# Performance work log

Measured on AMD Instinct MI355X. Metric: run time of the kernel, lower is better.

## Reference

```python
import jax, jax.numpy as jnp
import numpy as np

HID, PROJ, ATTN = 512, 1024, 128
B, L = 4, 2048


def _apply_rope(x):
    # x: [B, L, 2, ATTN]; RoPE over sequence dim (axis=1)
    half = x.shape[-1] // 2
    inv_freq = jnp.power(10000.0, -jnp.arange(half, dtype=jnp.float32) / half)
    pos = jnp.arange(x.shape[1], dtype=x.dtype)
    sinusoid = pos[:, None] * inv_freq.astype(x.dtype)          # [L, half]
    sin = jnp.sin(sinusoid)[None, :, None, :]                   # [1, L, 1, half]
    cos = jnp.cos(sinusoid)[None, :, None, :]
    x1, x2 = jnp.split(x, 2, axis=-1)
    return jnp.concatenate([x1 * cos - x2 * sin, x2 * cos + x1 * sin], axis=-1)


def setup_inputs() -> dict:
    key = jax.random.key(0)
    ks = jax.random.split(key, 8)
    node = jax.random.normal(ks[0], (B, L, HID), dtype=jnp.float32)
    bias = jax.random.normal(ks[1], (B, L, L), dtype=jnp.float32)
    scaling = jnp.full((1,), ATTN ** -0.5, dtype=jnp.float32)
    w1 = jax.random.normal(ks[2], (HID, 2 * PROJ + ATTN), dtype=jnp.float32) * (HID ** -0.5)
    b1 = jnp.zeros((2 * PROJ + ATTN,), dtype=jnp.float32)
    ms_weight = jax.random.normal(ks[3], (2, ATTN), dtype=jnp.float32) * 0.02
    ms_bias = jnp.zeros((2, ATTN), dtype=jnp.float32)
    w2 = jax.random.normal(ks[4], (PROJ, HID), dtype=jnp.float32) * (PROJ ** -0.5)
    b2 = jnp.zeros((HID,), dtype=jnp.float32)
    return {"node": node, "bias": bias, "scaling": scaling, "w1": w1, "b1": b1,
            "ms_weight": ms_weight, "ms_bias": ms_bias, "w2": w2, "b2": b2}


def reference(node, bias, scaling, w1, b1, ms_weight, ms_bias, w2, b2):
    # gated projection + SiLU
    gva = jax.nn.silu(node @ w1 + b1)                           # [B, L, 2P+A]
    gates, values, base = jnp.split(gva, [PROJ, 2 * PROJ], axis=-1)
    # multi-headed scaling -> [B, L, 2, A], then RoPE, then split q/k
    qk = base[..., None, :] * ms_weight + ms_bias               # [B, L, 2, A]
    qk = _apply_rope(qk)
    q, k = qk[..., 0, :], qk[..., 1, :]                         # [B, L, A]
    logits = jnp.einsum('bid,bjd->bij', q * scaling, k) + bias  # [B, L, L]
    attn = jax.nn.softmax(logits, axis=-1)
    out = jnp.einsum('bij,bjd->bid', attn, values)              # [B, L, P]
    return (out * gates) @ w2 + b2                              # [B, L, HID]
```

## Files before the change

### kernel.cpp

```cpp
#include <hip/hip_runtime.h>
#include <math.h>

#define HIDN 512
#define PROJ 1024
#define ATTN 128
#define BATCH 4
#define SEQ 2048
#define N1 (2*PROJ+ATTN)
#define ROWS (BATCH*SEQ)
#define QR 16

typedef __attribute__((ext_vector_type(4))) float f32x4;
typedef __attribute__((ext_vector_type(8))) short bf16x8;

__device__ __forceinline__ short f2bf(float x){
    unsigned u = __builtin_bit_cast(unsigned, x);
    unsigned rounding = 0x7fffu + ((u >> 16) & 1u);
    u += rounding;
    return (short)(u >> 16);
}
__device__ __forceinline__ float bf2f(short s){
    unsigned u = ((unsigned)(unsigned short)s) << 16;
    return __builtin_bit_cast(float, u);
}

__device__ __forceinline__ void gload16(const void* g, void* l){
    __builtin_amdgcn_global_load_lds((const __attribute__((address_space(1))) void*)g,
                                     (__attribute__((address_space(3))) void*)l,
                                     16, 0, 0);
}

template<class Epi>
__device__ __forceinline__ void gemm_bt_tile(const short* __restrict__ A, int lda,
                                             const short* __restrict__ BT, int ldb,
                                             int m0, int n0, int K, Epi epi)
{
    __shared__ __align__(16) short lA[2][128*64];
    __shared__ __align__(16) short lB[2][128*64];
    const int t = threadIdx.x;
    const int lane = t & 63;
    const int w = t >> 6;
    const int wr = (w >> 1) * 64, wc = (w & 1) * 64;
    const int half = lane >> 4, l16 = lane & 15;

    f32x4 acc[4][4];
    #pragma unroll
    for (int i=0;i<4;i++)
        #pragma unroll
        for (int j=0;j<4;j++)
            acc[i][j] = (f32x4){0.f,0.f,0.f,0.f};

    auto stage = [&](int buf, int k0){
        #pragma unroll
        for (int i = 0; i < 4; i++) {
            int li = i*256 + t;
            int r = li >> 3, s = li & 7;
            int ss = s ^ (r & 7);
            gload16(A + (size_t)(m0+r)*lda + k0 + ss*8, lA[buf] + li*8);
        }
        #pragma unroll
        for (int i = 0; i < 4; i++) {
            int li = i*256 + t;
            int r = li >> 3, s = li & 7;
            int ss = s ^ (r & 7);
            gload16(BT + (size_t)(n0+r)*ldb + k0 + ss*8, lB[buf] + li*8);
        }
    };

    stage(0, 0);
    __syncthreads();
    int cur = 0;
    for (int k0 = 64; k0 <= K; k0 += 64) {
        if (k0 < K) stage(cur^1, k0);
        #pragma unroll
        for (int kk = 0; kk < 64; kk += 32) {
            bf16x8 af[4], bfr[4];
            const int cs = (kk >> 3) + half;
            #pragma unroll
            for (int i=0;i<4;i++){
                int row = wr + i*16 + l16;
                af[i] = *(const bf16x8*)(lA[cur] + row*64 + ((cs ^ (row & 7)) << 3));
            }
            #pragma unroll
            for (int j=0;j<4;j++){
                int row = wc + j*16 + l16;
                bfr[j] = *(const bf16x8*)(lB[cur] + row*64 + ((cs ^ (row & 7)) << 3));
            }
            #pragma unroll
            for (int i=0;i<4;i++)
                #pragma unroll
                for (int j=0;j<4;j++)
                    acc[i][j] = __builtin_amdgcn_mfma_f32_16x16x32_bf16(af[i], bfr[j], acc[i][j], 0, 0, 0);
        }
        __syncthreads();
        cur ^= 1;
    }
    #pragma unroll
    for (int i=0;i<4;i++)
        #pragma unroll
        for (int j=0;j<4;j++)
            #pragma unroll
            for (int q=0;q<4;q++)
                epi(m0 + wr + i*16 + half*4 + q, n0 + wc + j*16 + l16, acc[i][j][q]);
}

__global__ void k_cast_node(const float* __restrict__ in, short* __restrict__ out){
    int idx = blockIdx.x*256 + threadIdx.x;
    const float4 v = ((const float4*)in)[idx];
    short4 o; o.x = f2bf(v.x); o.y = f2bf(v.y); o.z = f2bf(v.z); o.w = f2bf(v.w);
    ((short4*)out)[idx] = o;
}

__global__ void k_transpose_cast(const float* __restrict__ in, short* __restrict__ out,
                                 int R, int C){
    __shared__ short tile[64][65];
    int r0 = blockIdx.y*64, c0 = blockIdx.x*64;
    int t = threadIdx.x;
    #pragma unroll
    for (int i=0;i<16;i++){
        int lin = i*256 + t; int r = lin>>6, c = lin&63;
        tile[r][c] = f2bf(in[(size_t)(r0+r)*C + c0+c]);
    }
    __syncthreads();
    #pragma unroll
    for (int i=0;i<16;i++){
        int lin = i*256 + t; int c = lin>>6, r = lin&63;
        out[(size_t)(c0+c)*R + r0+r] = tile[r][c];
    }
}

__global__ void k_transpose_v(const short* __restrict__ values, short* __restrict__ VT){
    __shared__ short tile[64][65];
    int z = blockIdx.z;
    int c0 = blockIdx.x*64, r0 = blockIdx.y*64;
    int t = threadIdx.x;
    #pragma unroll
    for (int i=0;i<16;i++){
        int lin = i*256 + t; int r = lin>>6, c = lin&63;
        tile[r][c] = values[(size_t)(z*SEQ + r0+r)*PROJ + c0+c];
    }
    __syncthreads();
    #pragma unroll
    for (int i=0;i<16;i++){
        int lin = i*256 + t; int c = lin>>6, r = lin&63;
        VT[((size_t)z*PROJ + c0+c)*SEQ + r0+r] = tile[r][c];
    }
}

__global__ __launch_bounds__(256) void k_mm1(const short* __restrict__ nodeb,
        const short* __restrict__ w1T, const float* __restrict__ b1,
        short* __restrict__ gates, short* __restrict__ values, short* __restrict__ baseb){
    int b = blockIdx.x;
    int wg = (b & 7) * (N1/128*64/8) + (b >> 3);
    int n0 = (wg % (N1/128))*128, m0 = (wg / (N1/128))*128;
    gemm_bt_tile(nodeb, HIDN, w1T, HIDN, m0, n0, HIDN,
        [=](int row, int col, float v){
            v += b1[col];
            v = v / (1.f + __expf(-v));
            short bv = f2bf(v);
            if (col < PROJ)        gates [(size_t)row*PROJ + col]        = bv;
            else if (col < 2*PROJ) values[(size_t)row*PROJ + col-PROJ]   = bv;
            else                   baseb [(size_t)row*ATTN + col-2*PROJ] = bv;
        });
}

__global__ void k_rope2(const short* __restrict__ baseb, const float* __restrict__ msw,
                        const float* __restrict__ msb, const float* __restrict__ scaling,
                        short* __restrict__ qb, short* __restrict__ kb){
    int idx = blockIdx.x*256 + threadIdx.x;
    int d = idx & 63;
    int row = idx >> 6;
    int l = row & (SEQ-1);
    float inv = exp2f(-(float)d * (13.287712379549449f/64.f));
    float ang = (float)l * inv;
    float s = sinf(ang), c = cosf(ang);
    const short* bp = baseb + (size_t)row*ATTN;
    float b_lo = bf2f(bp[d]), b_hi = bf2f(bp[d+64]);
    float x1q = b_lo*msw[d]        + msb[d];
    float x2q = b_hi*msw[d+64]     + msb[d+64];
    float x1k = b_lo*msw[128+d]    + msb[128+d];
    float x2k = b_hi*msw[128+d+64] + msb[128+d+64];
    float sc = scaling[0];
    qb[(size_t)row*ATTN + d]    = f2bf((x1q*c - x2q*s)*sc);
    qb[(size_t)row*ATTN + d+64] = f2bf((x2q*c + x1q*s)*sc);
    kb[(size_t)row*ATTN + d]    = f2bf(x1k*c - x2k*s);
    kb[(size_t)row*ATTN + d+64] = f2bf(x2k*c + x1k*s);
}

__global__ __launch_bounds__(512, 4) void k_qksm(
        const short* __restrict__ qg, const short* __restrict__ kg,
        const float* __restrict__ bias, short* __restrict__ P,
        float* __restrict__ linv)
{
    __shared__ float bt[2][16][260];
    __shared__ short pt[2][16][264];
    __shared__ float s_l[8][16];

    const int z = blockIdx.y;
    const int r0 = blockIdx.x * QR;
    const int t = threadIdx.x;
    const int w = t >> 6;
    const int lane = t & 63;
    const int l16 = lane & 15, half = lane >> 4;

    const short* Q  = qg + ((size_t)z*SEQ + r0)*ATTN;
    const short* K  = kg + (size_t)z*SEQ*ATTN;
    const float* Bb = bias + ((size_t)z*SEQ + r0)*SEQ;
    short* Pp = P + ((size_t)z*SEQ + r0)*SEQ;

    bf16x8 qf[4];
    #pragma unroll
    for (int kc=0;kc<4;kc++)
        qf[kc] = *(const bf16x8*)(Q + (size_t)l16*ATTN + kc*32 + half*8);

    const int brow = t >> 6, bcol = (t & 63)*4;
    f32x4 pra[2], prb[2];
    pra[0] = *(const f32x4*)(Bb + (size_t)brow*SEQ + bcol);
    prb[0] = *(const f32x4*)(Bb + (size_t)(8+brow)*SEQ + bcol);
    pra[1] = *(const f32x4*)(Bb + (size_t)brow*SEQ + 256 + bcol);
    prb[1] = *(const f32x4*)(Bb + (size_t)(8+brow)*SEQ + 256 + bcol);
    *(f32x4*)&bt[0][brow][bcol]   = pra[0];
    *(f32x4*)&bt[0][8+brow][bcol] = prb[0];
    __syncthreads();

    float ts = 0.f;
    #pragma unroll
    for (int c=0; c<8; c++){
        const int cb = c & 1;
        if (c < 7){
            *(f32x4*)&bt[cb^1][brow][bcol]   = pra[(c+1)&1];
            *(f32x4*)&bt[cb^1][8+brow][bcol] = prb[(c+1)&1];
        }
        if (c < 6){
            pra[c&1] = *(const f32x4*)(Bb + (size_t)brow*SEQ + (c+2)*256 + bcol);
            prb[c&1] = *(const f32x4*)(Bb + (size_t)(8+brow)*SEQ + (c+2)*256 + bcol);
        }
        #pragma unroll
        for (int i=0;i<2;i++){
            int tile = w*2 + i;
            const short* Kc = K + (size_t)(c*256 + tile*16 + l16)*ATTN;
            f32x4 a = (f32x4){0.f,0.f,0.f,0.f};
            #pragma unroll
            for (int kc=0;kc<4;kc++){
                bf16x8 kf = *(const bf16x8*)(Kc + kc*32 + half*8);
                a = __builtin_amdgcn_mfma_f32_16x16x32_bf16(kf, qf[kc], a, 0,0,0);
            }
            a += *(const f32x4*)&bt[cb][l16][tile*16 + half*4];
            float p0 = __expf(a[0]), p1 = __expf(a[1]);
            float p2 = __expf(a[2]), p3 = __expf(a[3]);
            ts += p0+p1+p2+p3;
            unsigned u0 = (unsigned)(unsigned short)f2bf(p0) | ((unsigned)(unsigned short)f2bf(p1)<<16);
            unsigned u1 = (unsigned)(unsigned short)f2bf(p2) | ((unsigned)(unsigned short)f2bf(p3)<<16);
            short* pd = &pt[cb][l16][tile*16 + half*4];
            *(unsigned*)(pd)     = u0;
            *(unsigned*)(pd + 2) = u1;
        }
        if (c > 0){
            int row = t >> 5, colg = t & 31;
            *(bf16x8*)(Pp + (size_t)row*SEQ + (c-1)*256 + colg*8) =
                *(const bf16x8*)&pt[cb^1][row][colg*8];
        }
        __syncthreads();
    }
    {
        int row = t >> 5, colg = t & 31;
        *(bf16x8*)(Pp + (size_t)row*SEQ + 7*256 + colg*8) =
            *(const bf16x8*)&pt[1][row][colg*8];
    }
    ts += __shfl_xor(ts,16,64);
    ts += __shfl_xor(ts,32,64);
    if (half==0) s_l[w][l16] = ts;
    __syncthreads();
    if (w==0 && half==0){
        float sum = 0.f;
        #pragma unroll
        for (int ww=0; ww<8; ww++) sum += s_l[ww][l16];
        linv[(size_t)z*SEQ + r0 + l16] = 1.f/sum;
    }
}

__global__ __launch_bounds__(256) void k_pv2(const short* __restrict__ P,
        const short* __restrict__ VT, const short* __restrict__ gates,
        const float* __restrict__ linv, short* __restrict__ a2){
    int b = blockIdx.x;
    int wg = (b & 7) * 64 + (b >> 3);
    int xx = wg & 7, yy = (wg >> 3) & 15, z = wg >> 7;
    const short* A = P  + (size_t)z*SEQ*SEQ;
    const short* B = VT + (size_t)z*PROJ*SEQ;
    int n0 = xx*128, m0 = yy*128;
    gemm_bt_tile(A, SEQ, B, SEQ, m0, n0, SEQ,
        [=](int r, int c, float v){
            size_t gi = ((size_t)z*SEQ + r)*PROJ + c;
            a2[gi] = f2bf(v * linv[(size_t)z*SEQ + r] * bf2f(gates[gi]));
        });
}

__global__ __launch_bounds__(256) void k_mm2(const short* __restrict__ a2,
        const short* __restrict__ w2T, const float* __restrict__ b2,
        float* __restrict__ out){
    int b = blockIdx.x;
    int wg = (b & 7) * 32 + (b >> 3);
    int n0 = (wg & 3)*128, m0 = (wg >> 2)*128;
    gemm_bt_tile(a2, PROJ, w2T, PROJ, m0, n0, PROJ,
        [=](int r, int c, float v){
            out[(size_t)r*HIDN + c] = v + b2[c];
        });
}

extern "C" void kernel_launch(void* const* d_in, const int* in_sizes, int n_in,
                              void* d_out, int out_size, void* d_ws, size_t ws_size,
                              hipStream_t stream) {
    const float* node    = (const float*)d_in[0];
    const float* bias    = (const float*)d_in[1];
    const float* scaling = (const float*)d_in[2];
    const float* w1      = (const float*)d_in[3];
    const float* b1      = (const float*)d_in[4];
    const float* msw     = (const float*)d_in[5];
    const float* msb     = (const float*)d_in[6];
    const float* w2      = (const float*)d_in[7];
    const float* b2      = (const float*)d_in[8];
    float* out = (float*)d_out;

    char* p = (char*)d_ws;
    auto alloc = [&](size_t bytes){ char* r = p; p += (bytes + 255) & ~(size_t)255; return r; };
    short* nodeb  = (short*)alloc((size_t)ROWS*HIDN*2);
    short* w1T    = (short*)alloc((size_t)N1*HIDN*2);
    short* w2T    = (short*)alloc((size_t)HIDN*PROJ*2);
    short* gates  = (short*)alloc((size_t)ROWS*PROJ*2);
    short* values = (short*)alloc((size_t)ROWS*PROJ*2);
    short* VT     = (short*)alloc((size_t)BATCH*PROJ*SEQ*2);
    short* baseb  = (short*)alloc((size_t)ROWS*ATTN*2);
    short* qb     = (short*)alloc((size_t)ROWS*ATTN*2);
    short* kb     = (short*)alloc((size_t)ROWS*ATTN*2);
    short* Pbuf   = (short*)alloc((size_t)BATCH*SEQ*SEQ*2);
    float* linv   = (float*)alloc((size_t)ROWS*4);
    short* a2buf  = (short*)alloc((size_t)ROWS*PROJ*2);

    k_cast_node<<<ROWS*HIDN/1024, 256, 0, stream>>>(node, nodeb);
    k_transpose_cast<<<dim3(N1/64, HIDN/64), 256, 0, stream>>>(w1, w1T, HIDN, N1);
    k_transpose_cast<<<dim3(HIDN/64, PROJ/64), 256, 0, stream>>>(w2, w2T, PROJ, HIDN);
    k_mm1<<<(N1/128)*(ROWS/128), 256, 0, stream>>>(nodeb, w1T, b1, gates, values, baseb);
    k_transpose_v<<<dim3(PROJ/64, SEQ/64, BATCH), 256, 0, stream>>>(values, VT);
    k_rope2<<<ROWS*64/256, 256, 0, stream>>>(baseb, msw, msb, scaling, qb, kb);
    k_qksm<<<dim3(SEQ/QR, BATCH), 512, 0, stream>>>(qb, kb, bias, Pbuf, linv);
    k_pv2<<<(PROJ/128)*(SEQ/128)*BATCH, 256, 0, stream>>>(Pbuf, VT, gates, linv, a2buf);
    k_mm2<<<(HIDN/128)*(ROWS/128), 256, 0, stream>>>(a2buf, w2T, b2, out);
}
```

Before: 170.9 us.

## Template GEMM K-tile size and restructure QK softmax kernel to drop shared bias staging

The GEMM tile becomes templated on its K-step, with BK=32 and a matching LDS swizzle for the two projection GEMMs, while PV keeps 64; the smaller LDS footprint may allow more resident blocks. The QK/softmax kernel is rewritten so each wave loads its bias slice straight into the MFMA accumulator and prefetches the next chunk in registers. This removes the shared bias buffer and the per-chunk block barriers. Probabilities are now written through a small per-wave LDS tile and the row sums are reduced with lane shuffles. The bias loads become scalar strided reads, which may coalesce worse than the earlier vector loads.

```diff
diff --git a/kernel.cpp b/kernel.cpp
--- a/kernel.cpp
+++ b/kernel.cpp
@@ -30,18 +30,19 @@
                                      16, 0, 0);
 }
 
-template<class Epi>
+template<int BK, class Epi>
 __device__ __forceinline__ void gemm_bt_tile(const short* __restrict__ A, int lda,
                                              const short* __restrict__ BT, int ldb,
                                              int m0, int n0, int K, Epi epi)
 {
-    __shared__ __align__(16) short lA[2][128*64];
-    __shared__ __align__(16) short lB[2][128*64];
+    __shared__ __align__(16) short lA[2][128*BK];
+    __shared__ __align__(16) short lB[2][128*BK];
     const int t = threadIdx.x;
     const int lane = t & 63;
     const int w = t >> 6;
     const int wr = (w >> 1) * 64, wc = (w & 1) * 64;
     const int half = lane >> 4, l16 = lane & 15;
+    constexpr int SPT = BK/16;
 
     f32x4 acc[4][4];
     #pragma unroll
@@ -52,17 +53,17 @@
 
     auto stage = [&](int buf, int k0){
         #pragma unroll
-        for (int i = 0; i < 4; i++) {
+        for (int i = 0; i < SPT; i++) {
             int li = i*256 + t;
-            int r = li >> 3, s = li & 7;
-            int ss = s ^ (r & 7);
+            int r = li / (BK/8), s = li % (BK/8);
+            int ss = (BK==64) ? (s ^ (r & 7)) : (s ^ ((r >> 1) & 3));
             gload16(A + (size_t)(m0+r)*lda + k0 + ss*8, lA[buf] + li*8);
         }
         #pragma unroll
-        for (int i = 0; i < 4; i++) {
+        for (int i = 0; i < SPT; i++) {
             int li = i*256 + t;
-            int r = li >> 3, s = li & 7;
-            int ss = s ^ (r & 7);
+            int r = li / (BK/8), s = li % (BK/8);
+            int ss = (BK==64) ? (s ^ (r & 7)) : (s ^ ((r >> 1) & 3));
             gload16(BT + (size_t)(n0+r)*ldb + k0 + ss*8, lB[buf] + li*8);
         }
     };
@@ -70,21 +71,23 @@
     stage(0, 0);
     __syncthreads();
     int cur = 0;
-    for (int k0 = 64; k0 <= K; k0 += 64) {
+    for (int k0 = BK; k0 <= K; k0 += BK) {
         if (k0 < K) stage(cur^1, k0);
         #pragma unroll
-        for (int kk = 0; kk < 64; kk += 32) {
+        for (int kk = 0; kk < BK; kk += 32) {
             bf16x8 af[4], bfr[4];
             const int cs = (kk >> 3) + half;
             #pragma unroll
             for (int i=0;i<4;i++){
                 int row = wr + i*16 + l16;
-                af[i] = *(const bf16x8*)(lA[cur] + row*64 + ((cs ^ (row & 7)) << 3));
+                int sl = (BK==64) ? (cs ^ (row & 7)) : (cs ^ ((row >> 1) & 3));
+                af[i] = *(const bf16x8*)(lA[cur] + row*BK + sl*8);
             }
             #pragma unroll
             for (int j=0;j<4;j++){
                 int row = wc + j*16 + l16;
-                bfr[j] = *(const bf16x8*)(lB[cur] + row*64 + ((cs ^ (row & 7)) << 3));
+                int sl = (BK==64) ? (cs ^ (row & 7)) : (cs ^ ((row >> 1) & 3));
+                bfr[j] = *(const bf16x8*)(lB[cur] + row*BK + sl*8);
             }
             #pragma unroll
             for (int i=0;i<4;i++)
@@ -153,7 +156,7 @@
     int b = blockIdx.x;
     int wg = (b & 7) * (N1/128*64/8) + (b >> 3);
     int n0 = (wg % (N1/128))*128, m0 = (wg / (N1/128))*128;
-    gemm_bt_tile(nodeb, HIDN, w1T, HIDN, m0, n0, HIDN,
+    gemm_bt_tile<32>(nodeb, HIDN, w1T, HIDN, m0, n0, HIDN,
         [=](int row, int col, float v){
             v += b1[col];
             v = v / (1.f + __expf(-v));
@@ -192,8 +195,7 @@
         const float* __restrict__ bias, short* __restrict__ P,
         float* __restrict__ linv)
 {
-    __shared__ float bt[2][16][260];
-    __shared__ short pt[2][16][264];
+    __shared__ short ptw[8][16][56];
     __shared__ float s_l[8][16];
 
     const int z = blockIdx.y;
@@ -213,69 +215,71 @@
     for (int kc=0;kc<4;kc++)
         qf[kc] = *(const bf16x8*)(Q + (size_t)l16*ATTN + kc*32 + half*8);
 
-    const int brow = t >> 6, bcol = (t & 63)*4;
-    f32x4 pra[2], prb[2];
-    pra[0] = *(const f32x4*)(Bb + (size_t)brow*SEQ + bcol);
-    prb[0] = *(const f32x4*)(Bb + (size_t)(8+brow)*SEQ + bcol);
-    pra[1] = *(const f32x4*)(Bb + (size_t)brow*SEQ + 256 + bcol);
-    prb[1] = *(const f32x4*)(Bb + (size_t)(8+brow)*SEQ + 256 + bcol);
-    *(f32x4*)&bt[0][brow][bcol]   = pra[0];
-    *(f32x4*)&bt[0][8+brow][bcol] = prb[0];
-    __syncthreads();
-
-    float ts = 0.f;
-    #pragma unroll
+    f32x4 ts = (f32x4){0.f,0.f,0.f,0.f};
+
+    float bn[2][4];
+    #pragma unroll
+    for (int j=0;j<2;j++)
+        #pragma unroll
+        for (int e=0;e<4;e++)
+            bn[j][e] = Bb[(size_t)(half*4+e)*SEQ + w*32 + j*16 + l16];
+
+    #pragma unroll 2
     for (int c=0; c<8; c++){
-        const int cb = c & 1;
+        float bx[2][4];
         if (c < 7){
-            *(f32x4*)&bt[cb^1][brow][bcol]   = pra[(c+1)&1];
-            *(f32x4*)&bt[cb^1][8+brow][bcol] = prb[(c+1)&1];
-        }
-        if (c < 6){
-            pra[c&1] = *(const f32x4*)(Bb + (size_t)brow*SEQ + (c+2)*256 + bcol);
-            prb[c&1] = *(const f32x4*)(Bb + (size_t)(8+brow)*SEQ + (c+2)*256 + bcol);
-        }
-        #pragma unroll
-        for (int i=0;i<2;i++){
-            int tile = w*2 + i;
-            const short* Kc = K + (size_t)(c*256 + tile*16 + l16)*ATTN;
-            f32x4 a = (f32x4){0.f,0.f,0.f,0.f};
+            #pragma unroll
+            for (int j=0;j<2;j++)
+                #pragma unroll
+                for (int e=0;e<4;e++)
+                    bx[j][e] = Bb[(size_t)(half*4+e)*SEQ + (c+1)*256 + w*32 + j*16 + l16];
+        }
+        #pragma unroll
+        for (int j=0;j<2;j++){
+            const int kvb = c*256 + w*32 + j*16;
+            const short* Kc = K + (size_t)(kvb + l16)*ATTN;
+            f32x4 a = (f32x4){bn[j][0], bn[j][1], bn[j][2], bn[j][3]};
             #pragma unroll
             for (int kc=0;kc<4;kc++){
                 bf16x8 kf = *(const bf16x8*)(Kc + kc*32 + half*8);
-                a = __builtin_amdgcn_mfma_f32_16x16x32_bf16(kf, qf[kc], a, 0,0,0);
+                a = __builtin_amdgcn_mfma_f32_16x16x32_bf16(qf[kc], kf, a, 0,0,0);
             }
-            a += *(const f32x4*)&bt[cb][l16][tile*16 + half*4];
             float p0 = __expf(a[0]), p1 = __expf(a[1]);
             float p2 = __expf(a[2]), p3 = __expf(a[3]);
-            ts += p0+p1+p2+p3;
-            unsigned u0 = (unsigned)(unsigned short)f2bf(p0) | ((unsigned)(unsigned short)f2bf(p1)<<16);
-            unsigned u1 = (unsigned)(unsigned short)f2bf(p2) | ((unsigned)(unsigned short)f2bf(p3)<<16);
-            short* pd = &pt[cb][l16][tile*16 + half*4];
-            *(unsigned*)(pd)     = u0;
-            *(unsigned*)(pd + 2) = u1;
-        }
-        if (c > 0){
-            int row = t >> 5, colg = t & 31;
-            *(bf16x8*)(Pp + (size_t)row*SEQ + (c-1)*256 + colg*8) =
-                *(const bf16x8*)&pt[cb^1][row][colg*8];
-        }
-        __syncthreads();
-    }
-    {
-        int row = t >> 5, colg = t & 31;
-        *(bf16x8*)(Pp + (size_t)row*SEQ + 7*256 + colg*8) =
-            *(const bf16x8*)&pt[1][row][colg*8];
-    }
-    ts += __shfl_xor(ts,16,64);
-    ts += __shfl_xor(ts,32,64);
-    if (half==0) s_l[w][l16] = ts;
+            ts[0] += p0; ts[1] += p1; ts[2] += p2; ts[3] += p3;
+            ptw[w][half*4+0][j*16+l16] = f2bf(p0);
+            ptw[w][half*4+1][j*16+l16] = f2bf(p1);
+            ptw[w][half*4+2][j*16+l16] = f2bf(p2);
+            ptw[w][half*4+3][j*16+l16] = f2bf(p3);
+        }
+        {
+            bf16x8 v = *(const bf16x8*)&ptw[w][lane>>2][(lane&3)*8];
+            *(bf16x8*)(Pp + (size_t)(lane>>2)*SEQ + c*256 + w*32 + (lane&3)*8) = v;
+        }
+        #pragma unroll
+        for (int j=0;j<2;j++)
+            #pragma unroll
+            for (int e=0;e<4;e++)
+                bn[j][e] = bx[j][e];
+    }
+
+    #pragma unroll
+    for (int e=0;e<4;e++){
+        ts[e] += __shfl_xor(ts[e],1,64);
+        ts[e] += __shfl_xor(ts[e],2,64);
+        ts[e] += __shfl_xor(ts[e],4,64);
+        ts[e] += __shfl_xor(ts[e],8,64);
+    }
+    if (l16 == 0){
+        #pragma unroll
+        for (int e=0;e<4;e++) s_l[w][half*4+e] = ts[e];
+    }
     __syncthreads();
-    if (w==0 && half==0){
+    if (t < 16){
         float sum = 0.f;
         #pragma unroll
-        for (int ww=0; ww<8; ww++) sum += s_l[ww][l16];
-        linv[(size_t)z*SEQ + r0 + l16] = 1.f/sum;
+        for (int ww=0; ww<8; ww++) sum += s_l[ww][t];
+        linv[(size_t)z*SEQ + r0 + t] = 1.f/sum;
     }
 }
 
@@ -288,7 +292,7 @@
     const short* A = P  + (size_t)z*SEQ*SEQ;
     const short* B = VT + (size_t)z*PROJ*SEQ;
     int n0 = xx*128, m0 = yy*128;
-    gemm_bt_tile(A, SEQ, B, SEQ, m0, n0, SEQ,
+    gemm_bt_tile<64>(A, SEQ, B, SEQ, m0, n0, SEQ,
         [=](int r, int c, float v){
             size_t gi = ((size_t)z*SEQ + r)*PROJ + c;
             a2[gi] = f2bf(v * linv[(size_t)z*SEQ + r] * bf2f(gates[gi]));
@@ -301,7 +305,7 @@
     int b = blockIdx.x;
     int wg = (b & 7) * 32 + (b >> 3);
     int n0 = (wg & 3)*128, m0 = (wg >> 2)*128;
-    gemm_bt_tile(a2, PROJ, w2T, PROJ, m0, n0, PROJ,
+    gemm_bt_tile<32>(a2, PROJ, w2T, PROJ, m0, n0, PROJ,
         [=](int r, int c, float v){
             out[(size_t)r*HIDN + c] = v + b2[c];
         });
```

Result: faster. 164.8 us (-3.6%).
